# Performance work log

Measured on AMD Instinct MI355X. Metric: run time of the kernel, lower is better.

The kernel has to match this reference:

```python
import jax, jax.numpy as jnp
import numpy as np

B, DIM, T = 8, 1024, 4096
CB, CD = 4096, 8          # codebook_size, codebook_dim
COMMIT = 0.25
EPS = 1e-12


def _weight_norm(v, g):
    # torch weight_norm over dim=0: per-output-channel norm of v
    n = jnp.sqrt(jnp.sum(v * v, axis=1, keepdims=True))
    return g[:, None] * v / n


def _l2_normalize(x):
    n = jnp.sqrt(jnp.sum(x * x, axis=1, keepdims=True))
    return x / jnp.maximum(n, EPS)


def setup_inputs() -> dict:
    key = jax.random.key(0)
    ks = jax.random.split(key, 5)
    z = jax.random.normal(ks[0], (B, DIM, T), jnp.float32)
    v_in = jax.random.normal(ks[1], (CD, DIM), jnp.float32) * 0.02   # conv1d k=1 weight (squeezed)
    g_in = jnp.sqrt(jnp.sum(v_in * v_in, axis=1))                     # weight_norm init: g = ||v||
    b_in = jnp.zeros((CD,), jnp.float32)
    codebook = jax.random.normal(ks[2], (CB, CD), jnp.float32)        # nn.Embedding default N(0,1)
    v_out = jax.random.normal(ks[3], (DIM, CD), jnp.float32) * 0.02
    g_out = jnp.sqrt(jnp.sum(v_out * v_out, axis=1))
    b_out = jnp.zeros((DIM,), jnp.float32)
    return {"z": z, "v_in": v_in, "g_in": g_in, "b_in": b_in,
            "codebook": codebook, "v_out": v_out, "g_out": g_out, "b_out": b_out}


def reference(z, v_in, g_in, b_in, codebook, v_out, g_out, b_out):
    # in_proj: weight-normed 1x1 Conv1d == per-timestep matmul
    W_in = _weight_norm(v_in, g_in)                              # [CD, DIM]
    z_e = jnp.einsum('od,bdt->bot', W_in, z) + b_in[None, :, None]  # [B, CD, T]

    # decode_latents: normalize encodings and codebook, squared-L2 distances
    enc = z_e.transpose(0, 2, 1).reshape(B * T, CD)              # (b t) d
    e_n = _l2_normalize(enc)                                     # [BT, CD]
    c_n = _l2_normalize(codebook)                                # [CB, CD]
    dist = (jnp.sum(e_n * e_n, axis=1, keepdims=True)
            - 2.0 * (e_n @ c_n.T)
            + jnp.sum(c_n * c_n, axis=1)[None, :])               # [BT, CB]
    indices = jnp.argmin(dist, axis=1).reshape(B, T)             # [B, T] int

    # decode_code: gather UN-normalized codebook, transpose to [B, CD, T]
    z_q = codebook[indices].transpose(0, 2, 1)                   # [B, CD, T]

    # training losses (per-batch), commitment + codebook
    sg = jax.lax.stop_gradient
    commitment_loss = jnp.mean((z_e - sg(z_q)) ** 2, axis=(1, 2)) * COMMIT
    codebook_loss = jnp.mean((z_q - sg(z_e)) ** 2, axis=(1, 2))
    commit_loss = commitment_loss + codebook_loss                # [B]

    # straight-through estimator
    z_q_ste = z_e + sg(z_q - z_e)                                # [B, CD, T]

    # out_proj
    W_out = _weight_norm(v_out, g_out)                           # [DIM, CD]
    out = jnp.einsum('oc,bct->bot', W_out, z_q_ste) + b_out[None, :, None]  # [B, DIM, T]
    return out, indices, commit_loss
```

## Files before the change

### kernel.cpp

```cpp
#include <hip/hip_runtime.h>

#define DIMN 1024
#define TN 4096
#define BN 8
#define CBN 4096
#define CDN 8
#define BTN (BN*TN)
#define OUT_ELEMS (BN*DIMN*TN)

#define WS_WINT 0
#define WS_WOUT 8192
#define WS_CN   16384
#define WS_C2   49152
#define WS_ZE   53248
#define WS_IDX  315392
#define WS_LOSS 348160
#define WS_PART 348168

__device__ __forceinline__ float dot4(float4 a, float4 b) {
    float d = a.x * b.x;
    d = fmaf(a.y, b.y, d);
    d = fmaf(a.z, b.z, d);
    d = fmaf(a.w, b.w, d);
    return d;
}

__global__ __launch_bounds__(256) void k0_prep(
    const float* __restrict__ v_in, const float* __restrict__ g_in,
    const float* __restrict__ codebook, const float* __restrict__ v_out,
    const float* __restrict__ g_out, float* __restrict__ ws) {
    __shared__ float sred[5];
    int blk = blockIdx.x, tid = threadIdx.x;
    if (blk < 8) {
        int o = blk;
        const float* v = v_in + o * DIMN;
        float4 x = *(const float4*)(v + tid * 4);
        float p = x.x * x.x + x.y * x.y + x.z * x.z + x.w * x.w;
        for (int off = 32; off >= 1; off >>= 1) p += __shfl_down(p, off, 64);
        if ((tid & 63) == 0) sred[tid >> 6] = p;
        __syncthreads();
        if (tid == 0) {
            float tot = sred[0] + sred[1] + sred[2] + sred[3];
            sred[4] = g_in[o] / sqrtf(tot);
        }
        __syncthreads();
        float s = sred[4];
        ws[WS_WINT + (tid * 4 + 0) * 8 + o] = x.x * s;
        ws[WS_WINT + (tid * 4 + 1) * 8 + o] = x.y * s;
        ws[WS_WINT + (tid * 4 + 2) * 8 + o] = x.z * s;
        ws[WS_WINT + (tid * 4 + 3) * 8 + o] = x.w * s;
    } else if (blk < 12) {
        int r = (blk - 8) * 256 + tid;
        const float* v = v_out + r * 8;
        float4 a = *(const float4*)v;
        float4 b = *(const float4*)(v + 4);
        float n2 = dot4(a, a) + dot4(b, b);
        float s = g_out[r] / sqrtf(n2);
        *(float4*)(ws + WS_WOUT + r * 8)     = make_float4(a.x*s, a.y*s, a.z*s, a.w*s);
        *(float4*)(ws + WS_WOUT + r * 8 + 4) = make_float4(b.x*s, b.y*s, b.z*s, b.w*s);
    } else if (blk < 28) {
        int j = (blk - 12) * 256 + tid;
        const float* c = codebook + j * 8;
        float4 a = *(const float4*)c;
        float4 b = *(const float4*)(c + 4);
        float n2 = dot4(a, a) + dot4(b, b);
        float inv = 1.0f / fmaxf(sqrtf(n2), 1e-12f);
        float4 na = make_float4(a.x*inv, a.y*inv, a.z*inv, a.w*inv);
        float4 nb = make_float4(b.x*inv, b.y*inv, b.z*inv, b.w*inv);
        *(float4*)(ws + WS_CN + j * 8)     = na;
        *(float4*)(ws + WS_CN + j * 8 + 4) = nb;
        ws[WS_C2 + j] = -0.5f * (dot4(na, na) + dot4(nb, nb));
    } else {
        if (tid < 8) ws[WS_LOSS + tid] = 0.0f;
    }
}

__global__ __launch_bounds__(512) void k1a_ze(
    const float* __restrict__ z, const float* __restrict__ b_in,
    float* __restrict__ ws) {
    __shared__ float wlds[8192];
    __shared__ float plds[8 * 128 * 8];
    int tid = threadIdx.x, blk = blockIdx.x;
    int b = blk >> 5;
    int tt0 = (blk & 31) * 128;
    #pragma unroll
    for (int i = 0; i < 4; i++) {
        int f4 = tid + i * 512;
        *(float4*)(wlds + f4 * 4) = *(const float4*)(ws + WS_WINT + f4 * 4);
    }
    __syncthreads();
    int w = tid >> 6, lane = tid & 63;
    int d0 = w * 128;
    const float* zp = z + ((size_t)(b * DIMN + d0)) * TN + tt0 + lane * 2;
    float acc[16];
    #pragma unroll
    for (int i = 0; i < 16; i++) acc[i] = 0.0f;
    #pragma unroll 8
    for (int d = 0; d < 128; ++d) {
        float2 zv = *(const float2*)(zp + (size_t)d * TN);
        const float* wv = wlds + (d0 + d) * 8;
        #pragma unroll
        for (int c = 0; c < 8; c++) {
            float wc = wv[c];
            acc[c * 2]     = fmaf(wc, zv.x, acc[c * 2]);
            acc[c * 2 + 1] = fmaf(wc, zv.y, acc[c * 2 + 1]);
        }
    }
    float* pl = plds + (w * 128 + lane * 2) * 8;
    *(float4*)(pl)      = make_float4(acc[0], acc[2], acc[4], acc[6]);
    *(float4*)(pl + 4)  = make_float4(acc[8], acc[10], acc[12], acc[14]);
    *(float4*)(pl + 8)  = make_float4(acc[1], acc[3], acc[5], acc[7]);
    *(float4*)(pl + 12) = make_float4(acc[9], acc[11], acc[13], acc[15]);
    __syncthreads();
    int f0 = tid * 2;
    int t = f0 >> 3, c0 = f0 & 7;
    float2 s = make_float2(0.f, 0.f);
    #pragma unroll
    for (int w2 = 0; w2 < 8; w2++) {
        float2 p = *(float2*)(plds + (w2 * 128 + t) * 8 + c0);
        s.x += p.x; s.y += p.y;
    }
    s.x += b_in[c0]; s.y += b_in[c0 + 1];
    *(float2*)(ws + WS_ZE + (size_t)(b * TN + tt0 + t) * 8 + c0) = s;
}

__global__ __launch_bounds__(256) void k1b_search(float* __restrict__ ws) {
    __shared__ float cnL[1024 * 8];
    __shared__ float hL[1024];
    __shared__ float mbuf[128 * 2 * 2];
    int tid = threadIdx.x;
    int tile = blockIdx.x, q = blockIdx.y;
    int jbase = q * 1024;
    #pragma unroll
    for (int i = 0; i < 8; i++) {
        int f4 = tid + i * 256;
        *(float4*)(cnL + f4 * 4) = *(const float4*)(ws + WS_CN + (size_t)jbase * 8 + f4 * 4);
    }
    #pragma unroll
    for (int i = 0; i < 4; i++) {
        int o = tid + i * 256;
        hL[o] = ws[WS_C2 + jbase + o];
    }
    __syncthreads();
    int half = tid >> 7, tp = tid & 127;
    int t0 = tile * 256 + tp * 2;
    const float* zp = ws + WS_ZE + (size_t)t0 * 8;
    float4 za0 = *(const float4*)zp,        zb0 = *(const float4*)(zp + 4);
    float4 za1 = *(const float4*)(zp + 8),  zb1 = *(const float4*)(zp + 12);
    float inv0 = 1.0f / fmaxf(sqrtf(dot4(za0, za0) + dot4(zb0, zb0)), 1e-12f);
    float inv1 = 1.0f / fmaxf(sqrtf(dot4(za1, za1) + dot4(zb1, zb1)), 1e-12f);
    float4 ea0 = make_float4(za0.x*inv0, za0.y*inv0, za0.z*inv0, za0.w*inv0);
    float4 eb0 = make_float4(zb0.x*inv0, zb0.y*inv0, zb0.z*inv0, zb0.w*inv0);
    float4 ea1 = make_float4(za1.x*inv1, za1.y*inv1, za1.z*inv1, za1.w*inv1);
    float4 eb1 = make_float4(zb1.x*inv1, zb1.y*inv1, zb1.z*inv1, zb1.w*inv1);
    int j0 = half * 512;
    float bs0 = -3.4e38f, bs1 = -3.4e38f;
    int bi0 = 0, bi1 = 0;
    #pragma unroll 4
    for (int j = 0; j < 512; ++j) {
        const float* cr = cnL + (j0 + j) * 8;
        float4 ca = *(const float4*)cr;
        float4 cb = *(const float4*)(cr + 4);
        float hh = hL[j0 + j];
        float s0 = fmaf(ea0.x, ca.x, hh);
        s0 = fmaf(ea0.y, ca.y, s0); s0 = fmaf(ea0.z, ca.z, s0); s0 = fmaf(ea0.w, ca.w, s0);
        s0 = fmaf(eb0.x, cb.x, s0); s0 = fmaf(eb0.y, cb.y, s0);
        s0 = fmaf(eb0.z, cb.z, s0); s0 = fmaf(eb0.w, cb.w, s0);
        float s1 = fmaf(ea1.x, ca.x, hh);
        s1 = fmaf(ea1.y, ca.y, s1); s1 = fmaf(ea1.z, ca.z, s1); s1 = fmaf(ea1.w, ca.w, s1);
        s1 = fmaf(eb1.x, cb.x, s1); s1 = fmaf(eb1.y, cb.y, s1);
        s1 = fmaf(eb1.z, cb.z, s1); s1 = fmaf(eb1.w, cb.w, s1);
        if (s0 > bs0) { bs0 = s0; bi0 = j; }
        if (s1 > bs1) { bs1 = s1; bi1 = j; }
    }
    int gi0 = jbase + j0 + bi0, gi1 = jbase + j0 + bi1;
    float2* mb = (float2*)mbuf;
    if (half == 1) {
        mb[tp * 2]     = make_float2(bs0, __int_as_float(gi0));
        mb[tp * 2 + 1] = make_float2(bs1, __int_as_float(gi1));
    }
    __syncthreads();
    if (half == 0) {
        float2 o0 = mb[tp * 2], o1 = mb[tp * 2 + 1];
        if (o0.x > bs0) { bs0 = o0.x; gi0 = __float_as_int(o0.y); }
        if (o1.x > bs1) { bs1 = o1.x; gi1 = __float_as_int(o1.y); }
        *(float4*)(ws + WS_PART + ((size_t)q * 32768 + t0) * 2) =
            make_float4(bs0, __int_as_float(gi0), bs1, __int_as_float(gi1));
    }
}

__global__ __launch_bounds__(512) void k1c_merge(
    const float* __restrict__ codebook, float* __restrict__ ws) {
    int t = blockIdx.x * 512 + threadIdx.x;
    const float2* part = (const float2*)(ws + WS_PART);
    float2 p = part[t];
    float best = p.x; int bi = __float_as_int(p.y);
    #pragma unroll
    for (int q2 = 1; q2 < 4; q2++) {
        float2 pq = part[q2 * 32768 + t];
        if (pq.x > best) { best = pq.x; bi = __float_as_int(pq.y); }
    }
    ((int*)ws)[WS_IDX + t] = bi;
    const float* zep = ws + WS_ZE + (size_t)t * 8;
    float4 za = *(const float4*)zep, zb = *(const float4*)(zep + 4);
    const float* cq = codebook + (size_t)bi * 8;
    float4 qa = *(const float4*)cq, qb = *(const float4*)(cq + 4);
    float4 da = make_float4(za.x-qa.x, za.y-qa.y, za.z-qa.z, za.w-qa.w);
    float4 db = make_float4(zb.x-qb.x, zb.y-qb.y, zb.z-qb.z, zb.w-qb.w);
    float l = dot4(da, da) + dot4(db, db);
    for (int off = 32; off >= 1; off >>= 1) l += __shfl_down(l, off, 64);
    if ((threadIdx.x & 63) == 0) atomicAdd(ws + WS_LOSS + (t >> 12), l);
}

__global__ __launch_bounds__(256) void k2_out(
    const float* __restrict__ codebook, const float* __restrict__ b_out,
    float* __restrict__ dout, const float* __restrict__ ws) {
    __shared__ float zq[8 * 128];
    __shared__ float wl[256 * 8];
    __shared__ float bo_l[256];
    int tid = threadIdx.x, blk = blockIdx.x;
    int b = blk >> 7;
    int rem = blk & 127;
    int t0 = (rem >> 2) * 128;
    int o0 = (rem & 3) * 256;
    const int* wsi = (const int*)ws;
    {
        int pair = tid >> 1, halfq = tid & 1;
        int idx = wsi[WS_IDX + b * TN + t0 + pair] & (CBN - 1);
        const float* cp = codebook + (size_t)idx * 8 + halfq * 4;
        float4 q4 = *(const float4*)cp;
        int cb = halfq * 4;
        zq[(cb + 0) * 128 + pair] = q4.x;
        zq[(cb + 1) * 128 + pair] = q4.y;
        zq[(cb + 2) * 128 + pair] = q4.z;
        zq[(cb + 3) * 128 + pair] = q4.w;
    }
    bo_l[tid] = b_out[o0 + tid];
    #pragma unroll
    for (int i = 0; i < 2; i++) {
        int f4 = tid + i * 256;
        *(float4*)(wl + f4 * 4) = *(const float4*)(ws + WS_WOUT + o0 * 8 + f4 * 4);
    }
    __syncthreads();
    int t4 = tid & 31, osub = tid >> 5;
    int tq = t4 * 4;
    float4 zr[8];
    #pragma unroll
    for (int c = 0; c < 8; c++) zr[c] = *(float4*)(zq + c * 128 + tq);
    for (int k = 0; k < 32; k++) {
        int ol = osub * 32 + k;
        int o = o0 + ol;
        float4 wa = *(float4*)(wl + ol * 8);
        float4 wb = *(float4*)(wl + ol * 8 + 4);
        float bo = bo_l[ol];
        float4 acc = make_float4(bo, bo, bo, bo);
        float wc[8] = {wa.x, wa.y, wa.z, wa.w, wb.x, wb.y, wb.z, wb.w};
        #pragma unroll
        for (int c = 0; c < 8; c++) {
            acc.x = fmaf(wc[c], zr[c].x, acc.x);
            acc.y = fmaf(wc[c], zr[c].y, acc.y);
            acc.z = fmaf(wc[c], zr[c].z, acc.z);
            acc.w = fmaf(wc[c], zr[c].w, acc.w);
        }
        acc.x = fminf(fmaxf(acc.x, -8.f), 8.f);
        acc.y = fminf(fmaxf(acc.y, -8.f), 8.f);
        acc.z = fminf(fmaxf(acc.z, -8.f), 8.f);
        acc.w = fminf(fmaxf(acc.w, -8.f), 8.f);
        size_t off = ((size_t)(b * DIMN + o)) * TN + (size_t)(t0 + tq);
        *(float4*)(dout + off) = acc;
    }
}

__global__ __launch_bounds__(256) void k3_epi(
    float* __restrict__ dout, const float* __restrict__ ws) {
    int tid = threadIdx.x, blk = blockIdx.x;
    const int* wsi = (const int*)ws;
    size_t base = (size_t)OUT_ELEMS;
    int i0 = blk * 512 + tid;
    dout[base + (size_t)i0]       = (float)(wsi[WS_IDX + i0] & (CBN - 1));
    dout[base + (size_t)i0 + 256] = (float)(wsi[WS_IDX + i0 + 256] & (CBN - 1));
    if (blk == 0 && tid < 8) {
        float lv = ws[WS_LOSS + tid] * (1.25f / 32768.0f);
        dout[base + (size_t)BTN + (size_t)tid] = lv;
    }
}

extern "C" void kernel_launch(void* const* d_in, const int* in_sizes, int n_in,
                              void* d_out, int out_size, void* d_ws, size_t ws_size,
                              hipStream_t stream) {
    (void)in_sizes; (void)n_in; (void)out_size; (void)ws_size;
    const float* z        = (const float*)d_in[0];
    const float* v_in     = (const float*)d_in[1];
    const float* g_in     = (const float*)d_in[2];
    const float* b_in     = (const float*)d_in[3];
    const float* codebook = (const float*)d_in[4];
    const float* v_out    = (const float*)d_in[5];
    const float* g_out    = (const float*)d_in[6];
    const float* b_out    = (const float*)d_in[7];
    float* out            = (float*)d_out;
    float* ws             = (float*)d_ws;

    hipLaunchKernelGGL(k0_prep, dim3(29), dim3(256), 0, stream,
                       v_in, g_in, codebook, v_out, g_out, ws);
    hipLaunchKernelGGL(k1a_ze, dim3(256), dim3(512), 0, stream, z, b_in, ws);
    hipLaunchKernelGGL(k1b_search, dim3(128, 4), dim3(256), 0, stream, ws);
    hipLaunchKernelGGL(k1c_merge, dim3(64), dim3(512), 0, stream, codebook, ws);
    hipLaunchKernelGGL(k2_out, dim3(1024), dim3(256), 0, stream,
                       codebook, b_out, out, ws);
    hipLaunchKernelGGL(k3_epi, dim3(64), dim3(256), 0, stream, out, ws);
}
```

Baseline: 323.0 us.

## Split z_e projection into partial sums, reduce downstream, drop epilogue kernel

The input projection kernel now has each warp write its own partial sum over a 128-channel slice to workspace, using float4 nontemporal loads of z and 256-thread blocks. This removes the in-block LDS reduction and its extra barrier. The search and merge kernels each re-sum the 8 partials and add the bias themselves. The index output moves into the merge kernel and the loss write becomes an extra block of the output kernel, so the separate epilogue launch is gone, and the large output store is now nontemporal. The cost is more workspace traffic, since the partials are read twice (once by each of two kernels).

```diff
diff --git a/kernel.cpp b/kernel.cpp
--- a/kernel.cpp
+++ b/kernel.cpp
@@ -8,14 +8,16 @@
 #define BTN (BN*TN)
 #define OUT_ELEMS (BN*DIMN*TN)
 
+typedef float fx4 __attribute__((ext_vector_type(4)));
+
 #define WS_WINT 0
 #define WS_WOUT 8192
 #define WS_CN   16384
 #define WS_C2   49152
-#define WS_ZE   53248
-#define WS_IDX  315392
-#define WS_LOSS 348160
-#define WS_PART 348168
+#define WS_IDX  53248
+#define WS_LOSS 86016
+#define WS_PART 86024
+#define WS_ZEP  360448
 
 __device__ __forceinline__ float dot4(float4 a, float4 b) {
     float d = a.x * b.x;
@@ -23,6 +25,9 @@
     d = fmaf(a.z, b.z, d);
     d = fmaf(a.w, b.w, d);
     return d;
+}
+__device__ __forceinline__ void add4(float4& a, float4 b) {
+    a.x += b.x; a.y += b.y; a.z += b.z; a.w += b.w;
 }
 
 __global__ __launch_bounds__(256) void k0_prep(
@@ -75,56 +80,52 @@
     }
 }
 
-__global__ __launch_bounds__(512) void k1a_ze(
-    const float* __restrict__ z, const float* __restrict__ b_in,
-    float* __restrict__ ws) {
-    __shared__ float wlds[8192];
-    __shared__ float plds[8 * 128 * 8];
+__global__ __launch_bounds__(256) void k1a_ze(
+    const float* __restrict__ z, float* __restrict__ ws) {
+    __shared__ float wlds[512 * 8];
     int tid = threadIdx.x, blk = blockIdx.x;
     int b = blk >> 5;
-    int tt0 = (blk & 31) * 128;
+    int r = blk & 31;
+    int t0 = (r >> 1) * 256;
+    int dbase = (r & 1) * 512;
     #pragma unroll
     for (int i = 0; i < 4; i++) {
-        int f4 = tid + i * 512;
-        *(float4*)(wlds + f4 * 4) = *(const float4*)(ws + WS_WINT + f4 * 4);
+        int f4 = tid + i * 256;
+        *(float4*)(wlds + f4 * 4) = *(const float4*)(ws + WS_WINT + dbase * 8 + f4 * 4);
     }
     __syncthreads();
     int w = tid >> 6, lane = tid & 63;
-    int d0 = w * 128;
-    const float* zp = z + ((size_t)(b * DIMN + d0)) * TN + tt0 + lane * 2;
-    float acc[16];
-    #pragma unroll
-    for (int i = 0; i < 16; i++) acc[i] = 0.0f;
+    const float* zp = z + ((size_t)(b * DIMN + dbase + w * 128)) * TN + t0 + lane * 4;
+    float4 acc[8];
+    #pragma unroll
+    for (int c = 0; c < 8; c++) acc[c] = make_float4(0.f, 0.f, 0.f, 0.f);
     #pragma unroll 8
-    for (int d = 0; d < 128; ++d) {
-        float2 zv = *(const float2*)(zp + (size_t)d * TN);
-        const float* wv = wlds + (d0 + d) * 8;
+    for (int dd = 0; dd < 128; ++dd) {
+        fx4 zr = __builtin_nontemporal_load((const fx4*)(zp + (size_t)dd * TN));
+        const float* wv = wlds + (w * 128 + dd) * 8;
         #pragma unroll
         for (int c = 0; c < 8; c++) {
             float wc = wv[c];
-            acc[c * 2]     = fmaf(wc, zv.x, acc[c * 2]);
-            acc[c * 2 + 1] = fmaf(wc, zv.y, acc[c * 2 + 1]);
+            acc[c].x = fmaf(wc, zr.x, acc[c].x);
+            acc[c].y = fmaf(wc, zr.y, acc[c].y);
+            acc[c].z = fmaf(wc, zr.z, acc[c].z);
+            acc[c].w = fmaf(wc, zr.w, acc[c].w);
         }
     }
-    float* pl = plds + (w * 128 + lane * 2) * 8;
-    *(float4*)(pl)      = make_float4(acc[0], acc[2], acc[4], acc[6]);
-    *(float4*)(pl + 4)  = make_float4(acc[8], acc[10], acc[12], acc[14]);
-    *(float4*)(pl + 8)  = make_float4(acc[1], acc[3], acc[5], acc[7]);
-    *(float4*)(pl + 12) = make_float4(acc[9], acc[11], acc[13], acc[15]);
-    __syncthreads();
-    int f0 = tid * 2;
-    int t = f0 >> 3, c0 = f0 & 7;
-    float2 s = make_float2(0.f, 0.f);
-    #pragma unroll
-    for (int w2 = 0; w2 < 8; w2++) {
-        float2 p = *(float2*)(plds + (w2 * 128 + t) * 8 + c0);
-        s.x += p.x; s.y += p.y;
-    }
-    s.x += b_in[c0]; s.y += b_in[c0 + 1];
-    *(float2*)(ws + WS_ZE + (size_t)(b * TN + tt0 + t) * 8 + c0) = s;
-}
-
-__global__ __launch_bounds__(256) void k1b_search(float* __restrict__ ws) {
+    int p = (r & 1) * 4 + w;
+    float* op = ws + WS_ZEP + ((size_t)p * BTN + b * TN + t0 + lane * 4) * 8;
+    *(float4*)(op +  0) = make_float4(acc[0].x, acc[1].x, acc[2].x, acc[3].x);
+    *(float4*)(op +  4) = make_float4(acc[4].x, acc[5].x, acc[6].x, acc[7].x);
+    *(float4*)(op +  8) = make_float4(acc[0].y, acc[1].y, acc[2].y, acc[3].y);
+    *(float4*)(op + 12) = make_float4(acc[4].y, acc[5].y, acc[6].y, acc[7].y);
+    *(float4*)(op + 16) = make_float4(acc[0].z, acc[1].z, acc[2].z, acc[3].z);
+    *(float4*)(op + 20) = make_float4(acc[4].z, acc[5].z, acc[6].z, acc[7].z);
+    *(float4*)(op + 24) = make_float4(acc[0].w, acc[1].w, acc[2].w, acc[3].w);
+    *(float4*)(op + 28) = make_float4(acc[4].w, acc[5].w, acc[6].w, acc[7].w);
+}
+
+__global__ __launch_bounds__(256) void k1b_search(
+    const float* __restrict__ b_in, float* __restrict__ ws) {
     __shared__ float cnL[1024 * 8];
     __shared__ float hL[1024];
     __shared__ float mbuf[128 * 2 * 2];
@@ -141,12 +142,20 @@
         int o = tid + i * 256;
         hL[o] = ws[WS_C2 + jbase + o];
     }
-    __syncthreads();
     int half = tid >> 7, tp = tid & 127;
     int t0 = tile * 256 + tp * 2;
-    const float* zp = ws + WS_ZE + (size_t)t0 * 8;
-    float4 za0 = *(const float4*)zp,        zb0 = *(const float4*)(zp + 4);
-    float4 za1 = *(const float4*)(zp + 8),  zb1 = *(const float4*)(zp + 12);
+    float4 bi0 = *(const float4*)(b_in);
+    float4 bi1 = *(const float4*)(b_in + 4);
+    float4 za0 = bi0, zb0 = bi1, za1 = bi0, zb1 = bi1;
+    #pragma unroll
+    for (int p = 0; p < 8; p++) {
+        const float* pp = ws + WS_ZEP + ((size_t)p * BTN + t0) * 8;
+        add4(za0, *(const float4*)(pp));
+        add4(zb0, *(const float4*)(pp + 4));
+        add4(za1, *(const float4*)(pp + 8));
+        add4(zb1, *(const float4*)(pp + 12));
+    }
+    __syncthreads();
     float inv0 = 1.0f / fmaxf(sqrtf(dot4(za0, za0) + dot4(zb0, zb0)), 1e-12f);
     float inv1 = 1.0f / fmaxf(sqrtf(dot4(za1, za1) + dot4(zb1, zb1)), 1e-12f);
     float4 ea0 = make_float4(za0.x*inv0, za0.y*inv0, za0.z*inv0, za0.w*inv0);
@@ -155,7 +164,7 @@
     float4 eb1 = make_float4(zb1.x*inv1, zb1.y*inv1, zb1.z*inv1, zb1.w*inv1);
     int j0 = half * 512;
     float bs0 = -3.4e38f, bs1 = -3.4e38f;
-    int bi0 = 0, bi1 = 0;
+    int bi = 0, bj = 0;
     #pragma unroll 4
     for (int j = 0; j < 512; ++j) {
         const float* cr = cnL + (j0 + j) * 8;
@@ -170,10 +179,10 @@
         s1 = fmaf(ea1.y, ca.y, s1); s1 = fmaf(ea1.z, ca.z, s1); s1 = fmaf(ea1.w, ca.w, s1);
         s1 = fmaf(eb1.x, cb.x, s1); s1 = fmaf(eb1.y, cb.y, s1);
         s1 = fmaf(eb1.z, cb.z, s1); s1 = fmaf(eb1.w, cb.w, s1);
-        if (s0 > bs0) { bs0 = s0; bi0 = j; }
-        if (s1 > bs1) { bs1 = s1; bi1 = j; }
-    }
-    int gi0 = jbase + j0 + bi0, gi1 = jbase + j0 + bi1;
+        if (s0 > bs0) { bs0 = s0; bi = j; }
+        if (s1 > bs1) { bs1 = s1; bj = j; }
+    }
+    int gi0 = jbase + j0 + bi, gi1 = jbase + j0 + bj;
     float2* mb = (float2*)mbuf;
     if (half == 1) {
         mb[tp * 2]     = make_float2(bs0, __int_as_float(gi0));
@@ -190,7 +199,8 @@
 }
 
 __global__ __launch_bounds__(512) void k1c_merge(
-    const float* __restrict__ codebook, float* __restrict__ ws) {
+    const float* __restrict__ codebook, const float* __restrict__ b_in,
+    float* __restrict__ dout, float* __restrict__ ws) {
     int t = blockIdx.x * 512 + threadIdx.x;
     const float2* part = (const float2*)(ws + WS_PART);
     float2 p = part[t];
@@ -201,8 +211,15 @@
         if (pq.x > best) { best = pq.x; bi = __float_as_int(pq.y); }
     }
     ((int*)ws)[WS_IDX + t] = bi;
-    const float* zep = ws + WS_ZE + (size_t)t * 8;
-    float4 za = *(const float4*)zep, zb = *(const float4*)(zep + 4);
+    dout[(size_t)OUT_ELEMS + t] = (float)bi;
+    float4 za = *(const float4*)(b_in);
+    float4 zb = *(const float4*)(b_in + 4);
+    #pragma unroll
+    for (int pi = 0; pi < 8; pi++) {
+        const float* pp = ws + WS_ZEP + ((size_t)pi * BTN + t) * 8;
+        add4(za, *(const float4*)(pp));
+        add4(zb, *(const float4*)(pp + 4));
+    }
     const float* cq = codebook + (size_t)bi * 8;
     float4 qa = *(const float4*)cq, qb = *(const float4*)(cq + 4);
     float4 da = make_float4(za.x-qa.x, za.y-qa.y, za.z-qa.z, za.w-qa.w);
@@ -219,6 +236,13 @@
     __shared__ float wl[256 * 8];
     __shared__ float bo_l[256];
     int tid = threadIdx.x, blk = blockIdx.x;
+    if (blk == 1024) {
+        if (tid < 8) {
+            float lv = ws[WS_LOSS + tid] * (1.25f / 32768.0f);
+            dout[(size_t)OUT_ELEMS + BTN + tid] = lv;
+        }
+        return;
+    }
     int b = blk >> 7;
     int rem = blk & 127;
     int t0 = (rem >> 2) * 128;
@@ -267,21 +291,8 @@
         acc.z = fminf(fmaxf(acc.z, -8.f), 8.f);
         acc.w = fminf(fmaxf(acc.w, -8.f), 8.f);
         size_t off = ((size_t)(b * DIMN + o)) * TN + (size_t)(t0 + tq);
-        *(float4*)(dout + off) = acc;
-    }
-}
-
-__global__ __launch_bounds__(256) void k3_epi(
-    float* __restrict__ dout, const float* __restrict__ ws) {
-    int tid = threadIdx.x, blk = blockIdx.x;
-    const int* wsi = (const int*)ws;
-    size_t base = (size_t)OUT_ELEMS;
-    int i0 = blk * 512 + tid;
-    dout[base + (size_t)i0]       = (float)(wsi[WS_IDX + i0] & (CBN - 1));
-    dout[base + (size_t)i0 + 256] = (float)(wsi[WS_IDX + i0 + 256] & (CBN - 1));
-    if (blk == 0 && tid < 8) {
-        float lv = ws[WS_LOSS + tid] * (1.25f / 32768.0f);
-        dout[base + (size_t)BTN + (size_t)tid] = lv;
+        fx4 st; st.x = acc.x; st.y = acc.y; st.z = acc.z; st.w = acc.w;
+        __builtin_nontemporal_store(st, (fx4*)(dout + off));
     }
 }
 
@@ -302,10 +313,10 @@
 
     hipLaunchKernelGGL(k0_prep, dim3(29), dim3(256), 0, stream,
                        v_in, g_in, codebook, v_out, g_out, ws);
-    hipLaunchKernelGGL(k1a_ze, dim3(256), dim3(512), 0, stream, z, b_in, ws);
-    hipLaunchKernelGGL(k1b_search, dim3(128, 4), dim3(256), 0, stream, ws);
-    hipLaunchKernelGGL(k1c_merge, dim3(64), dim3(512), 0, stream, codebook, ws);
-    hipLaunchKernelGGL(k2_out, dim3(1024), dim3(256), 0, stream,
+    hipLaunchKernelGGL(k1a_ze, dim3(256), dim3(256), 0, stream, z, ws);
+    hipLaunchKernelGGL(k1b_search, dim3(128, 4), dim3(256), 0, stream, b_in, ws);
+    hipLaunchKernelGGL(k1c_merge, dim3(64), dim3(512), 0, stream,
+                       codebook, b_in, out, ws);
+    hipLaunchKernelGGL(k2_out, dim3(1025), dim3(256), 0, stream,
                        codebook, b_out, out, ws);
-    hipLaunchKernelGGL(k3_epi, dim3(64), dim3(256), 0, stream, out, ws);
-}
+}
```

Result: no change. 318.4 us (-1.4%).
